# Kernel optimization log

Hardware: AMD Instinct MI355X
Metric: run time of the kernel (lower is better)

Reference implementation:

```python
import jax, jax.numpy as jnp
import numpy as np
import math

HIDDEN = 512
NUM_HEADS = 8
HEAD_DIM = HIDDEN // NUM_HEADS
NUM_BUCKETS = 32
MAX_DISTANCE = 128


def _relative_position_bucket(rel_pos, bidirectional=True):
    # rel_pos: int32 [S, T]
    num_buckets = NUM_BUCKETS
    ret = 0
    if bidirectional:
        num_buckets //= 2
        ret = (rel_pos > 0).astype(jnp.int32) * num_buckets
        rel_pos = jnp.abs(rel_pos)
    else:
        rel_pos = -jnp.minimum(rel_pos, 0)
    max_exact = num_buckets // 2
    is_small = rel_pos < max_exact
    # guard log(0); result unused where is_small
    safe = jnp.maximum(rel_pos, 1).astype(jnp.float32)
    val_if_large = max_exact + (
        jnp.log(safe / max_exact) / math.log(MAX_DISTANCE / max_exact) * (num_buckets - max_exact)
    ).astype(jnp.int32)
    val_if_large = jnp.minimum(val_if_large, num_buckets - 1)
    return ret + jnp.where(is_small, rel_pos, val_if_large)


def setup_inputs() -> dict:
    key = jax.random.key(0)
    ks = jax.random.split(key, 6)
    B, S = 4, 2048
    std = 1.0 / math.sqrt(HIDDEN)
    inp = {
        "x": jax.random.normal(ks[0], (B, S, HIDDEN), dtype=jnp.float32),
        "Wq": jax.random.normal(ks[1], (HIDDEN, HIDDEN), dtype=jnp.float32) * std,
        "Wk": jax.random.normal(ks[2], (HIDDEN, HIDDEN), dtype=jnp.float32) * std,
        "Wv": jax.random.normal(ks[3], (HIDDEN, HIDDEN), dtype=jnp.float32) * std,
        "Wo": jax.random.normal(ks[4], (HIDDEN, HIDDEN), dtype=jnp.float32) * std,
        "bias_table": jax.random.normal(ks[5], (NUM_BUCKETS, NUM_HEADS), dtype=jnp.float32) * 0.02,
    }
    return inp


def reference(x, Wq, Wk, Wv, Wo, bias_table):
    # x: [B, S, HIDDEN]; weights: [HIDDEN, HIDDEN] (out = x @ W.T semantics folded as x @ W here
    # -- weights are random so orientation is a convention; we use x @ W).
    B, S, _ = x.shape
    T = S  # self-attention, context=None
    scale = HEAD_DIM ** -0.5

    def split_heads(t, L):
        return t.reshape(B, L, NUM_HEADS, HEAD_DIM).transpose(0, 2, 1, 3)  # [B,H,L,D]

    q = split_heads(x @ Wq, S)
    k = split_heads(x @ Wk, T)
    v = split_heads(x @ Wv, T)

    # relative position bias: [1, H, S, T]
    rel = jnp.arange(T, dtype=jnp.int32)[None, :] - jnp.arange(S, dtype=jnp.int32)[:, None]
    buckets = _relative_position_bucket(rel, bidirectional=True)  # [S, T]
    pos_bias = bias_table[buckets]  # [S, T, H]
    pos_bias = pos_bias.transpose(2, 0, 1)[None]  # [1, H, S, T]

    attn = jnp.einsum("bhsd,bhtd->bhst", q, k) * scale + pos_bias
    attn = jax.nn.softmax(attn, axis=-1)  # dropout = identity (eval)
    out = jnp.einsum("bhst,bhtd->bhsd", attn, v)
    out = out.transpose(0, 2, 1, 3).reshape(B, S, HIDDEN)
    return out @ Wo
```

## Files before the change

kernel.cpp:

```cpp
#include <hip/hip_runtime.h>
#include <hip/hip_bf16.h>
#include <math.h>

#define HIDDEN 512
#define NHEADS 8
#define HDIM 64
#define SLEN 2048
#define BATCH 4
#define NROWS (BATCH*SLEN)
#define RTAB (2*SLEN-1)
#define LOG2E 1.44269504088896340736f
#define SCALE_L2E (0.125f * LOG2E)

typedef _Float16 f16;
typedef f16 f16x8 __attribute__((ext_vector_type(8)));
typedef float f32x4 __attribute__((ext_vector_type(4)));
typedef unsigned short u16;
typedef unsigned int u32;
typedef u16 u16x4 __attribute__((ext_vector_type(4)));
typedef u16 u16x8 __attribute__((ext_vector_type(8)));
typedef u32 u32x4 __attribute__((ext_vector_type(4)));

__global__ __launch_bounds__(256) void bias_precompute(
    const float* __restrict__ bias_table, float* __restrict__ biasrel) {
  int i = blockIdx.x * 256 + threadIdx.x;
  if (i >= NHEADS * RTAB) return;
  int h = i / RTAB;
  int idx = i - h * RTAB;
  int rel = idx - (SLEN - 1);
  int ret = rel > 0 ? 16 : 0;
  int a = rel < 0 ? -rel : rel;
  int bidx;
  if (a < 8) {
    bidx = a;
  } else {
    float val = logf((float)a * 0.125f) / logf(16.0f) * 8.0f;
    bidx = 8 + (int)val;
    if (bidx > 15) bidx = 15;
  }
  biasrel[i] = bias_table[(ret + bidx) * NHEADS + h] * LOG2E;
}

__global__ __launch_bounds__(256) void conv_x(
    const float* __restrict__ x, u16* __restrict__ xh) {
  int i = blockIdx.x * 256 + threadIdx.x;
  const float4* p = (const float4*)(x + (size_t)i * 8);
  float4 a = p[0], b = p[1];
  u16x8 o;
  f16 t0 = (f16)a.x; o[0] = *(u16*)&t0;
  f16 t1 = (f16)a.y; o[1] = *(u16*)&t1;
  f16 t2 = (f16)a.z; o[2] = *(u16*)&t2;
  f16 t3 = (f16)a.w; o[3] = *(u16*)&t3;
  f16 t4 = (f16)b.x; o[4] = *(u16*)&t4;
  f16 t5 = (f16)b.y; o[5] = *(u16*)&t5;
  f16 t6 = (f16)b.z; o[6] = *(u16*)&t6;
  f16 t7 = (f16)b.w; o[7] = *(u16*)&t7;
  *(u16x8*)(xh + (size_t)i * 8) = o;
}

__global__ __launch_bounds__(256) void conv_w(
    const float* __restrict__ Wq, const float* __restrict__ Wk,
    const float* __restrict__ Wv, const float* __restrict__ Wo,
    u16* __restrict__ Wt) {
  const float* W = blockIdx.y == 0 ? Wq : blockIdx.y == 1 ? Wk
                 : blockIdx.y == 2 ? Wv : Wo;
  u16* dst = Wt + (size_t)blockIdx.y * HIDDEN * HIDDEN;
  int t = blockIdx.x * 256 + threadIdx.x;
  int k = t >> 6, n0 = (t & 63) << 3;
  const float4* p = (const float4*)(W + (size_t)k * HIDDEN + n0);
  float4 a = p[0], b = p[1];
  float vals[8] = {a.x, a.y, a.z, a.w, b.x, b.y, b.z, b.w};
#pragma unroll
  for (int j = 0; j < 8; ++j) {
    f16 hv = (f16)vals[j];
    dst[(size_t)(n0 + j) * HIDDEN + k] = *(u16*)&hv;
  }
}

__global__ __launch_bounds__(256) void gemm_mfma(
    const u16* __restrict__ A, const u16* __restrict__ Wt0,
    const u16* __restrict__ Wt1, const u16* __restrict__ Wt2,
    void* __restrict__ O, int mode) {
  __shared__ u16 sm[2 * 128 * 72];
  u16 (*As)[72] = (u16(*)[72])sm;
  u16 (*Bs)[72] = (u16(*)[72])(sm + 128 * 72);
  const u16* Wt = blockIdx.z == 0 ? Wt0 : blockIdx.z == 1 ? Wt1 : Wt2;
  const int tid = threadIdx.x;
  const int w = tid >> 6, l = tid & 63;
  const int lr = l & 15, lg = l >> 4;
  const int wr = w >> 1, wc = w & 1;
  const int m0 = blockIdx.x << 7, n0 = blockIdx.y << 7;
  const int vtmode = (mode == 1) && (blockIdx.z == 2);

  f32x4 acc[4][4] = {};

  u16x8 areg[4], breg[4];
#pragma unroll
  for (int e = 0; e < 4; ++e) {
    int c = (e << 8) + tid;
    int row = c >> 3, g = c & 7;
    areg[e] = *(const u16x8*)(A + (size_t)(m0 + row) * HIDDEN + (g << 3));
    breg[e] = *(const u16x8*)(Wt + (size_t)(n0 + row) * HIDDEN + (g << 3));
  }

  for (int k0 = 0; k0 < HIDDEN; k0 += 64) {
    __syncthreads();
#pragma unroll
    for (int e = 0; e < 4; ++e) {
      int c = (e << 8) + tid;
      int row = c >> 3, g = c & 7;
      *(u16x8*)&As[row][g << 3] = areg[e];
      *(u16x8*)&Bs[row][g << 3] = breg[e];
    }
    __syncthreads();
    if (k0 + 64 < HIDDEN) {
#pragma unroll
      for (int e = 0; e < 4; ++e) {
        int c = (e << 8) + tid;
        int row = c >> 3, g = c & 7;
        areg[e] = *(const u16x8*)(A + (size_t)(m0 + row) * HIDDEN + k0 + 64 + (g << 3));
        breg[e] = *(const u16x8*)(Wt + (size_t)(n0 + row) * HIDDEN + k0 + 64 + (g << 3));
      }
    }
#pragma unroll
    for (int kk = 0; kk < 64; kk += 32) {
      f16x8 af[4], bf[4];
#pragma unroll
      for (int mt = 0; mt < 4; ++mt)
        af[mt] = *(const f16x8*)&As[(wr << 6) + (mt << 4) + lr][kk + (lg << 3)];
#pragma unroll
      for (int nt = 0; nt < 4; ++nt)
        bf[nt] = *(const f16x8*)&Bs[(wc << 6) + (nt << 4) + lr][kk + (lg << 3)];
      if (!vtmode) {
#pragma unroll
        for (int mt = 0; mt < 4; ++mt)
#pragma unroll
          for (int nt = 0; nt < 4; ++nt)
            acc[mt][nt] = __builtin_amdgcn_mfma_f32_16x16x32_f16(
                af[mt], bf[nt], acc[mt][nt], 0, 0, 0);
      } else {
#pragma unroll
        for (int i = 0; i < 4; ++i)
#pragma unroll
          for (int j = 0; j < 4; ++j)
            acc[i][j] = __builtin_amdgcn_mfma_f32_16x16x32_f16(
                bf[i], af[j], acc[i][j], 0, 0, 0);
      }
    }
  }

  if (mode == 0) {
    float* Of = (float*)O;
#pragma unroll
    for (int mt = 0; mt < 4; ++mt)
#pragma unroll
      for (int nt = 0; nt < 4; ++nt)
#pragma unroll
        for (int r = 0; r < 4; ++r) {
          int m = m0 + (wr << 6) + (mt << 4) + (lg << 2) + r;
          int n = n0 + (wc << 6) + (nt << 4) + lr;
          Of[(size_t)m * HIDDEN + n] = acc[mt][nt][r];
        }
  } else if (!vtmode) {
    u16* O16 = (u16*)O + (size_t)blockIdx.z * NROWS * HIDDEN;
    const float osc = (blockIdx.z == 0) ? SCALE_L2E : 1.0f;
#pragma unroll
    for (int mt = 0; mt < 4; ++mt)
#pragma unroll
      for (int nt = 0; nt < 4; ++nt)
#pragma unroll
        for (int r = 0; r < 4; ++r) {
          int m = m0 + (wr << 6) + (mt << 4) + (lg << 2) + r;
          int n = n0 + (wc << 6) + (nt << 4) + lr;
          int b = m >> 11, s = m & (SLEN - 1);
          int h = n >> 6, d = n & 63;
          f16 hv = (f16)(acc[mt][nt][r] * osc);
          O16[(((size_t)b * NHEADS + h) * SLEN + s) * HDIM + d] = *(u16*)&hv;
        }
  } else {
    __syncthreads();
    u16* tt = sm;
#pragma unroll
    for (int i = 0; i < 4; ++i)
#pragma unroll
      for (int j = 0; j < 4; ++j)
#pragma unroll
        for (int r = 0; r < 4; ++r) {
          int nl = (wc << 6) + (i << 4) + (lg << 2) + r;
          int ml = (wr << 6) + (j << 4) + lr;
          f16 hv = (f16)acc[i][j][r];
          tt[nl * 136 + ml] = *(u16*)&hv;
        }
    __syncthreads();
    u16* O16 = (u16*)O + (size_t)2 * NROWS * HIDDEN;
    int nl = tid >> 1, half = tid & 1;
    int n = n0 + nl;
    int h = n >> 6, d = n & 63;
    int b = m0 >> 11, s_base = m0 & (SLEN - 1);
    u16* orow = O16 + (((size_t)b * NHEADS + h) * HDIM + d) * SLEN + s_base;
    const u16* trow = tt + nl * 136;
#pragma unroll
    for (int c = 0; c < 8; ++c) {
      int v_off = (half << 6) + (c << 3);
      int c0 = (v_off & ~31) | (((v_off >> 3) & 3) << 2);
      u16x4 lo = *(const u16x4*)(trow + c0);
      u16x4 hi = *(const u16x4*)(trow + c0 + 16);
      u16x8 st;
#pragma unroll
      for (int j = 0; j < 4; ++j) { st[j] = lo[j]; st[j + 4] = hi[j]; }
      *(u16x8*)(orow + v_off) = st;
    }
  }
}

__global__ __launch_bounds__(256) void flash_attn_mfma(
    const u16* __restrict__ qg, const u16* __restrict__ kg,
    const u16* __restrict__ vtg, const float* __restrict__ biasrel,
    u16* __restrict__ attn_out) {
  __shared__ u16 Ks[64][72];
  __shared__ u16 Vt[64][72];

  const int tid = threadIdx.x;
  const int w = tid >> 6, l = tid & 63;
  const int lr = l & 15, lg = l >> 4;

  int bid = blockIdx.x;
  int xcd = bid & 7, idx = bid >> 3;
  int bh = (xcd << 2) + (idx >> 4);
  int bx = idx & 15;
  int h = bh & 7, b = bh >> 3;
  int q0 = bx << 7;

  const u16* qp = qg + (size_t)bh * (SLEN * HDIM);
  const u16* kp = kg + (size_t)bh * (SLEN * HDIM);
  const u16* vp = vtg + (size_t)bh * (HDIM * SLEN);

  const float bias_pos = biasrel[h * RTAB + 2 * (SLEN - 1)];
  const float bias_neg = biasrel[h * RTAB];

  f16x8 aq[2][2];
#pragma unroll
  for (int sub = 0; sub < 2; ++sub) {
    const u16* qrow = qp + (size_t)(q0 + (w << 5) + (sub << 4) + lr) * HDIM + (lg << 3);
    aq[sub][0] = *(const f16x8*)(qrow);
    aq[sub][1] = *(const f16x8*)(qrow + 32);
  }

  const float* bb = biasrel + h * RTAB + (SLEN - 1) + (lg << 2) - lr - q0 - (w << 5);

  f32x4 acc[2][4] = {};
  float l_run[2] = {0.f, 0.f};

  u16x8 kreg[2], vreg[2];
#pragma unroll
  for (int e = 0; e < 2; ++e) {
    int c = tid + (e << 8);
    int row = c >> 3, c8 = (c & 7) << 3;
    kreg[e] = *(const u16x8*)(kp + (size_t)row * HDIM + c8);
    vreg[e] = *(const u16x8*)(vp + (size_t)row * SLEN + c8);
  }

  for (int t0 = 0; t0 < SLEN; t0 += 64) {
    __syncthreads();
#pragma unroll
    for (int e = 0; e < 2; ++e) {
      int c = tid + (e << 8);
      int row = c >> 3, c8 = (c & 7) << 3;
      *(u16x8*)&Ks[row][c8] = kreg[e];
      *(u16x8*)&Vt[row][c8] = vreg[e];
    }
    __syncthreads();

    if (t0 + 64 < SLEN) {
#pragma unroll
      for (int e = 0; e < 2; ++e) {
        int c = tid + (e << 8);
        int row = c >> 3, c8 = (c & 7) << 3;
        kreg[e] = *(const u16x8*)(kp + (size_t)(t0 + 64 + row) * HDIM + c8);
        vreg[e] = *(const u16x8*)(vp + (size_t)row * SLEN + t0 + 64 + c8);
      }
    }

    int dtq = t0 - q0;
    f32x4 sc[2][4];
    if (dtq >= 256 || dtq <= -192) {
      float c = (dtq > 0) ? bias_pos : bias_neg;
      f32x4 cv = {c, c, c, c};
#pragma unroll
      for (int sub = 0; sub < 2; ++sub)
#pragma unroll
        for (int ct = 0; ct < 4; ++ct) sc[sub][ct] = cv;
    } else {
#pragma unroll
      for (int sub = 0; sub < 2; ++sub)
#pragma unroll
        for (int ct = 0; ct < 4; ++ct)
#pragma unroll
          for (int r = 0; r < 4; ++r)
            sc[sub][ct][r] = bb[t0 + (ct << 4) + r - (sub << 4)];
    }

    f16x8 kf[4][2];
#pragma unroll
    for (int ct = 0; ct < 4; ++ct) {
      kf[ct][0] = *(const f16x8*)&Ks[(ct << 4) + lr][lg << 3];
      kf[ct][1] = *(const f16x8*)&Ks[(ct << 4) + lr][32 + (lg << 3)];
    }

    __builtin_amdgcn_s_setprio(1);
#pragma unroll
    for (int sub = 0; sub < 2; ++sub)
#pragma unroll
      for (int ct = 0; ct < 4; ++ct) {
        sc[sub][ct] = __builtin_amdgcn_mfma_f32_16x16x32_f16(
            kf[ct][0], aq[sub][0], sc[sub][ct], 0, 0, 0);
        sc[sub][ct] = __builtin_amdgcn_mfma_f32_16x16x32_f16(
            kf[ct][1], aq[sub][1], sc[sub][ct], 0, 0, 0);
      }
    __builtin_amdgcn_s_setprio(0);

#pragma unroll
    for (int sub = 0; sub < 2; ++sub) {
      float rs = 0.f;
#pragma unroll
      for (int ct = 0; ct < 4; ++ct)
#pragma unroll
        for (int r = 0; r < 4; ++r) {
          float pe = __builtin_amdgcn_exp2f(sc[sub][ct][r]);
          sc[sub][ct][r] = pe;
          rs += pe;
        }
      l_run[sub] += rs;
    }

    f16x8 vf[2][4];
#pragma unroll
    for (int kb = 0; kb < 2; ++kb)
#pragma unroll
      for (int dt = 0; dt < 4; ++dt)
        vf[kb][dt] = *(const f16x8*)&Vt[(dt << 4) + lr][(kb << 5) + (lg << 3)];

    __builtin_amdgcn_s_setprio(1);
#pragma unroll
    for (int sub = 0; sub < 2; ++sub)
#pragma unroll
      for (int kb = 0; kb < 2; ++kb) {
        u32 a0 = __builtin_bit_cast(u32,
            __builtin_amdgcn_cvt_pkrtz(sc[sub][2 * kb][0], sc[sub][2 * kb][1]));
        u32 a1 = __builtin_bit_cast(u32,
            __builtin_amdgcn_cvt_pkrtz(sc[sub][2 * kb][2], sc[sub][2 * kb][3]));
        u32 a2 = __builtin_bit_cast(u32,
            __builtin_amdgcn_cvt_pkrtz(sc[sub][2 * kb + 1][0], sc[sub][2 * kb + 1][1]));
        u32 a3 = __builtin_bit_cast(u32,
            __builtin_amdgcn_cvt_pkrtz(sc[sub][2 * kb + 1][2], sc[sub][2 * kb + 1][3]));
        u32x4 pk = {a0, a1, a2, a3};
        f16x8 pa = __builtin_bit_cast(f16x8, pk);
#pragma unroll
        for (int dt = 0; dt < 4; ++dt)
          acc[sub][dt] = __builtin_amdgcn_mfma_f32_16x16x32_f16(
              pa, vf[kb][dt], acc[sub][dt], 0, 0, 0);
      }
    __builtin_amdgcn_s_setprio(0);
  }

#pragma unroll
  for (int sub = 0; sub < 2; ++sub) {
    float lt = l_run[sub];
    lt += __shfl_xor(lt, 16, 64);
    lt += __shfl_xor(lt, 32, 64);
    float linv[4];
#pragma unroll
    for (int r = 0; r < 4; ++r) linv[r] = 1.f / __shfl(lt, (lg << 2) + r, 16);
    u16* op = attn_out +
              ((size_t)(b * SLEN) + q0 + (w << 5) + (sub << 4)) * HIDDEN + (h << 6);
#pragma unroll
    for (int r = 0; r < 4; ++r)
#pragma unroll
      for (int dt = 0; dt < 4; ++dt) {
        f16 hv = (f16)(acc[sub][dt][r] * linv[r]);
        op[(size_t)((lg << 2) + r) * HIDDEN + (dt << 4) + lr] = *(u16*)&hv;
      }
  }
}

extern "C" void kernel_launch(void* const* d_in, const int* in_sizes, int n_in,
                              void* d_out, int out_size, void* d_ws, size_t ws_size,
                              hipStream_t stream) {
  const float* x          = (const float*)d_in[0];
  const float* Wq         = (const float*)d_in[1];
  const float* Wk         = (const float*)d_in[2];
  const float* Wv         = (const float*)d_in[3];
  const float* Wo         = (const float*)d_in[4];
  const float* bias_table = (const float*)d_in[5];
  float* out = (float*)d_out;

  u16* xh   = (u16*)d_ws;
  u16* wt   = xh + (size_t)NROWS * HIDDEN;
  u16* qkv  = wt + (size_t)4 * HIDDEN * HIDDEN;
  u16* attno_h = qkv + (size_t)3 * NROWS * HIDDEN;
  float* biasrel = (float*)(attno_h + (size_t)NROWS * HIDDEN);

  u16* qb = qkv;
  u16* kb = qkv + (size_t)NROWS * HIDDEN;
  u16* vb = qkv + (size_t)2 * NROWS * HIDDEN;

  bias_precompute<<<(NHEADS * RTAB + 255) / 256, 256, 0, stream>>>(bias_table, biasrel);
  conv_x<<<NROWS * HIDDEN / 8 / 256, 256, 0, stream>>>(x, xh);
  conv_w<<<dim3(HIDDEN * HIDDEN / 8 / 256, 4), 256, 0, stream>>>(Wq, Wk, Wv, Wo, wt);

  u16* wtq = wt;
  u16* wtk = wt + (size_t)HIDDEN * HIDDEN;
  u16* wtv = wt + (size_t)2 * HIDDEN * HIDDEN;
  u16* wto = wt + (size_t)3 * HIDDEN * HIDDEN;

  gemm_mfma<<<dim3(NROWS / 128, HIDDEN / 128, 3), 256, 0, stream>>>(
      xh, wtq, wtk, wtv, qkv, 1);

  flash_attn_mfma<<<SLEN / 128 * BATCH * NHEADS, 256, 0, stream>>>(
      qb, kb, vb, biasrel, attno_h);

  gemm_mfma<<<dim3(NROWS / 128, HIDDEN / 128, 1), 256, 0, stream>>>(
      attno_h, wto, wto, wto, out, 0);
}
```

Measured before the change: 105.3 us.

## Fuse x conversion into QKV GEMM, stage epilogue via LDS, double-buffer attention K/V

Removes the separate fp32-to-fp16 conversion kernel for x: the QKV GEMM now loads fp32 x and packs it with cvt_pkrtz on the fly. The Q scale is folded into the weight conversion. The Q/K epilogue is staged through shared memory so head-major stores are 16-byte vectors instead of scattered 2-byte writes. The flash attention K/V tiles are double-buffered in LDS, leaving one barrier per iteration. In exchange the QKV GEMM reads twice the A bytes from global memory across three z-slices, and attention uses more LDS per block.

```diff
diff --git a/kernel.cpp b/kernel.cpp
--- a/kernel.cpp
+++ b/kernel.cpp
@@ -20,6 +20,15 @@
 typedef u16 u16x4 __attribute__((ext_vector_type(4)));
 typedef u16 u16x8 __attribute__((ext_vector_type(8)));
 typedef u32 u32x4 __attribute__((ext_vector_type(4)));
+
+__device__ __forceinline__ u16x8 pack8(float4 a, float4 b) {
+  u32 p0 = __builtin_bit_cast(u32, __builtin_amdgcn_cvt_pkrtz(a.x, a.y));
+  u32 p1 = __builtin_bit_cast(u32, __builtin_amdgcn_cvt_pkrtz(a.z, a.w));
+  u32 p2 = __builtin_bit_cast(u32, __builtin_amdgcn_cvt_pkrtz(b.x, b.y));
+  u32 p3 = __builtin_bit_cast(u32, __builtin_amdgcn_cvt_pkrtz(b.z, b.w));
+  u32x4 r = {p0, p1, p2, p3};
+  return __builtin_bit_cast(u16x8, r);
+}
 
 __global__ __launch_bounds__(256) void bias_precompute(
     const float* __restrict__ bias_table, float* __restrict__ biasrel) {
@@ -41,29 +50,13 @@
   biasrel[i] = bias_table[(ret + bidx) * NHEADS + h] * LOG2E;
 }
 
-__global__ __launch_bounds__(256) void conv_x(
-    const float* __restrict__ x, u16* __restrict__ xh) {
-  int i = blockIdx.x * 256 + threadIdx.x;
-  const float4* p = (const float4*)(x + (size_t)i * 8);
-  float4 a = p[0], b = p[1];
-  u16x8 o;
-  f16 t0 = (f16)a.x; o[0] = *(u16*)&t0;
-  f16 t1 = (f16)a.y; o[1] = *(u16*)&t1;
-  f16 t2 = (f16)a.z; o[2] = *(u16*)&t2;
-  f16 t3 = (f16)a.w; o[3] = *(u16*)&t3;
-  f16 t4 = (f16)b.x; o[4] = *(u16*)&t4;
-  f16 t5 = (f16)b.y; o[5] = *(u16*)&t5;
-  f16 t6 = (f16)b.z; o[6] = *(u16*)&t6;
-  f16 t7 = (f16)b.w; o[7] = *(u16*)&t7;
-  *(u16x8*)(xh + (size_t)i * 8) = o;
-}
-
 __global__ __launch_bounds__(256) void conv_w(
     const float* __restrict__ Wq, const float* __restrict__ Wk,
     const float* __restrict__ Wv, const float* __restrict__ Wo,
     u16* __restrict__ Wt) {
   const float* W = blockIdx.y == 0 ? Wq : blockIdx.y == 1 ? Wk
                  : blockIdx.y == 2 ? Wv : Wo;
+  const float sc = (blockIdx.y == 0) ? SCALE_L2E : 1.0f;
   u16* dst = Wt + (size_t)blockIdx.y * HIDDEN * HIDDEN;
   int t = blockIdx.x * 256 + threadIdx.x;
   int k = t >> 6, n0 = (t & 63) << 3;
@@ -72,18 +65,20 @@
   float vals[8] = {a.x, a.y, a.z, a.w, b.x, b.y, b.z, b.w};
 #pragma unroll
   for (int j = 0; j < 8; ++j) {
-    f16 hv = (f16)vals[j];
+    f16 hv = (f16)(vals[j] * sc);
     dst[(size_t)(n0 + j) * HIDDEN + k] = *(u16*)&hv;
   }
 }
 
 __global__ __launch_bounds__(256) void gemm_mfma(
-    const u16* __restrict__ A, const u16* __restrict__ Wt0,
+    const void* __restrict__ Ap, const u16* __restrict__ Wt0,
     const u16* __restrict__ Wt1, const u16* __restrict__ Wt2,
     void* __restrict__ O, int mode) {
   __shared__ u16 sm[2 * 128 * 72];
   u16 (*As)[72] = (u16(*)[72])sm;
   u16 (*Bs)[72] = (u16(*)[72])(sm + 128 * 72);
+  const u16* A16 = (const u16*)Ap;
+  const float* A32 = (const float*)Ap;
   const u16* Wt = blockIdx.z == 0 ? Wt0 : blockIdx.z == 1 ? Wt1 : Wt2;
   const int tid = threadIdx.x;
   const int w = tid >> 6, l = tid & 63;
@@ -99,7 +94,12 @@
   for (int e = 0; e < 4; ++e) {
     int c = (e << 8) + tid;
     int row = c >> 3, g = c & 7;
-    areg[e] = *(const u16x8*)(A + (size_t)(m0 + row) * HIDDEN + (g << 3));
+    if (mode == 1) {
+      const float* ap = A32 + (size_t)(m0 + row) * HIDDEN + (g << 3);
+      areg[e] = pack8(*(const float4*)ap, *(const float4*)(ap + 4));
+    } else {
+      areg[e] = *(const u16x8*)(A16 + (size_t)(m0 + row) * HIDDEN + (g << 3));
+    }
     breg[e] = *(const u16x8*)(Wt + (size_t)(n0 + row) * HIDDEN + (g << 3));
   }
 
@@ -118,7 +118,12 @@
       for (int e = 0; e < 4; ++e) {
         int c = (e << 8) + tid;
         int row = c >> 3, g = c & 7;
-        areg[e] = *(const u16x8*)(A + (size_t)(m0 + row) * HIDDEN + k0 + 64 + (g << 3));
+        if (mode == 1) {
+          const float* ap = A32 + (size_t)(m0 + row) * HIDDEN + k0 + 64 + (g << 3);
+          areg[e] = pack8(*(const float4*)ap, *(const float4*)(ap + 4));
+        } else {
+          areg[e] = *(const u16x8*)(A16 + (size_t)(m0 + row) * HIDDEN + k0 + 64 + (g << 3));
+        }
         breg[e] = *(const u16x8*)(Wt + (size_t)(n0 + row) * HIDDEN + k0 + 64 + (g << 3));
       }
     }
@@ -162,21 +167,32 @@
           Of[(size_t)m * HIDDEN + n] = acc[mt][nt][r];
         }
   } else if (!vtmode) {
+    __syncthreads();
+    u16* tt = sm;
+#pragma unroll
+    for (int mt = 0; mt < 4; ++mt)
+#pragma unroll
+      for (int nt = 0; nt < 4; ++nt)
+#pragma unroll
+        for (int r = 0; r < 4; ++r) {
+          int ml = (wr << 6) + (mt << 4) + (lg << 2) + r;
+          int nl = (wc << 6) + (nt << 4) + lr;
+          f16 hv = (f16)acc[mt][nt][r];
+          tt[ml * 136 + nl] = *(u16*)&hv;
+        }
+    __syncthreads();
     u16* O16 = (u16*)O + (size_t)blockIdx.z * NROWS * HIDDEN;
-    const float osc = (blockIdx.z == 0) ? SCALE_L2E : 1.0f;
-#pragma unroll
-    for (int mt = 0; mt < 4; ++mt)
-#pragma unroll
-      for (int nt = 0; nt < 4; ++nt)
-#pragma unroll
-        for (int r = 0; r < 4; ++r) {
-          int m = m0 + (wr << 6) + (mt << 4) + (lg << 2) + r;
-          int n = n0 + (wc << 6) + (nt << 4) + lr;
-          int b = m >> 11, s = m & (SLEN - 1);
-          int h = n >> 6, d = n & 63;
-          f16 hv = (f16)(acc[mt][nt][r] * osc);
-          O16[(((size_t)b * NHEADS + h) * SLEN + s) * HDIM + d] = *(u16*)&hv;
-        }
+    int b = m0 >> 11, s0 = m0 & (SLEN - 1);
+    int hl = tid >> 7, rr = tid & 127;
+    int hh = (n0 >> 6) + hl;
+    u16* obase = O16 + (((size_t)b * NHEADS + hh) * SLEN + s0) * HDIM;
+#pragma unroll
+    for (int c = 0; c < 8; ++c) {
+      int sl = (rr >> 3) + (c << 4);
+      int d8 = (rr & 7) << 3;
+      u16x8 v = *(const u16x8*)&tt[sl * 136 + (hl << 6) + d8];
+      *(u16x8*)(obase + (size_t)sl * HDIM + d8) = v;
+    }
   } else {
     __syncthreads();
     u16* tt = sm;
@@ -217,8 +233,8 @@
     const u16* __restrict__ qg, const u16* __restrict__ kg,
     const u16* __restrict__ vtg, const float* __restrict__ biasrel,
     u16* __restrict__ attn_out) {
-  __shared__ u16 Ks[64][72];
-  __shared__ u16 Vt[64][72];
+  __shared__ u16 Ks[2][64][72];
+  __shared__ u16 Vt[2][64][72];
 
   const int tid = threadIdx.x;
   const int w = tid >> 6, l = tid & 63;
@@ -259,25 +275,40 @@
     kreg[e] = *(const u16x8*)(kp + (size_t)row * HDIM + c8);
     vreg[e] = *(const u16x8*)(vp + (size_t)row * SLEN + c8);
   }
-
+#pragma unroll
+  for (int e = 0; e < 2; ++e) {
+    int c = tid + (e << 8);
+    int row = c >> 3, c8 = (c & 7) << 3;
+    *(u16x8*)&Ks[0][row][c8] = kreg[e];
+    *(u16x8*)&Vt[0][row][c8] = vreg[e];
+  }
+#pragma unroll
+  for (int e = 0; e < 2; ++e) {
+    int c = tid + (e << 8);
+    int row = c >> 3, c8 = (c & 7) << 3;
+    kreg[e] = *(const u16x8*)(kp + (size_t)(64 + row) * HDIM + c8);
+    vreg[e] = *(const u16x8*)(vp + (size_t)row * SLEN + 64 + c8);
+  }
+  __syncthreads();
+
+  int cur = 0;
   for (int t0 = 0; t0 < SLEN; t0 += 64) {
-    __syncthreads();
-#pragma unroll
-    for (int e = 0; e < 2; ++e) {
-      int c = tid + (e << 8);
-      int row = c >> 3, c8 = (c & 7) << 3;
-      *(u16x8*)&Ks[row][c8] = kreg[e];
-      *(u16x8*)&Vt[row][c8] = vreg[e];
-    }
-    __syncthreads();
-
     if (t0 + 64 < SLEN) {
 #pragma unroll
       for (int e = 0; e < 2; ++e) {
         int c = tid + (e << 8);
         int row = c >> 3, c8 = (c & 7) << 3;
-        kreg[e] = *(const u16x8*)(kp + (size_t)(t0 + 64 + row) * HDIM + c8);
-        vreg[e] = *(const u16x8*)(vp + (size_t)row * SLEN + t0 + 64 + c8);
+        *(u16x8*)&Ks[cur ^ 1][row][c8] = kreg[e];
+        *(u16x8*)&Vt[cur ^ 1][row][c8] = vreg[e];
+      }
+      if (t0 + 128 < SLEN) {
+#pragma unroll
+        for (int e = 0; e < 2; ++e) {
+          int c = tid + (e << 8);
+          int row = c >> 3, c8 = (c & 7) << 3;
+          kreg[e] = *(const u16x8*)(kp + (size_t)(t0 + 128 + row) * HDIM + c8);
+          vreg[e] = *(const u16x8*)(vp + (size_t)row * SLEN + t0 + 128 + c8);
+        }
       }
     }
 
@@ -303,8 +334,8 @@
     f16x8 kf[4][2];
 #pragma unroll
     for (int ct = 0; ct < 4; ++ct) {
-      kf[ct][0] = *(const f16x8*)&Ks[(ct << 4) + lr][lg << 3];
-      kf[ct][1] = *(const f16x8*)&Ks[(ct << 4) + lr][32 + (lg << 3)];
+      kf[ct][0] = *(const f16x8*)&Ks[cur][(ct << 4) + lr][lg << 3];
+      kf[ct][1] = *(const f16x8*)&Ks[cur][(ct << 4) + lr][32 + (lg << 3)];
     }
 
     __builtin_amdgcn_s_setprio(1);
@@ -338,7 +369,7 @@
     for (int kb = 0; kb < 2; ++kb)
 #pragma unroll
       for (int dt = 0; dt < 4; ++dt)
-        vf[kb][dt] = *(const f16x8*)&Vt[(dt << 4) + lr][(kb << 5) + (lg << 3)];
+        vf[kb][dt] = *(const f16x8*)&Vt[cur][(dt << 4) + lr][(kb << 5) + (lg << 3)];
 
     __builtin_amdgcn_s_setprio(1);
 #pragma unroll
@@ -361,6 +392,9 @@
               pa, vf[kb][dt], acc[sub][dt], 0, 0, 0);
       }
     __builtin_amdgcn_s_setprio(0);
+
+    __syncthreads();
+    cur ^= 1;
   }
 
 #pragma unroll
@@ -394,8 +428,7 @@
   const float* bias_table = (const float*)d_in[5];
   float* out = (float*)d_out;
 
-  u16* xh   = (u16*)d_ws;
-  u16* wt   = xh + (size_t)NROWS * HIDDEN;
+  u16* wt   = (u16*)d_ws;
   u16* qkv  = wt + (size_t)4 * HIDDEN * HIDDEN;
   u16* attno_h = qkv + (size_t)3 * NROWS * HIDDEN;
   float* biasrel = (float*)(attno_h + (size_t)NROWS * HIDDEN);
@@ -405,7 +438,6 @@
   u16* vb = qkv + (size_t)2 * NROWS * HIDDEN;
 
   bias_precompute<<<(NHEADS * RTAB + 255) / 256, 256, 0, stream>>>(bias_table, biasrel);
-  conv_x<<<NROWS * HIDDEN / 8 / 256, 256, 0, stream>>>(x, xh);
   conv_w<<<dim3(HIDDEN * HIDDEN / 8 / 256, 4), 256, 0, stream>>>(Wq, Wk, Wv, Wo, wt);
 
   u16* wtq = wt;
@@ -414,7 +446,7 @@
   u16* wto = wt + (size_t)3 * HIDDEN * HIDDEN;
 
   gemm_mfma<<<dim3(NROWS / 128, HIDDEN / 128, 3), 256, 0, stream>>>(
-      xh, wtq, wtk, wtv, qkv, 1);
+      x, wtq, wtk, wtv, qkv, 1);
 
   flash_attn_mfma<<<SLEN / 128 * BATCH * NHEADS, 256, 0, stream>>>(
       qb, kb, vb, biasrel, attno_h);
```

New measurement: 127.5 us. 1.21x slower.

## Double-buffer K/V tiles in LDS to drop one barrier per iteration

Applied to the files above, without the earlier changes.

Adds a second LDS buffer for the K and V tiles. Each iteration writes the next tile into the alternate buffer while computing on the current one, which leaves one __syncthreads per iteration instead of two. The global prefetch now runs two tiles ahead. In exchange the LDS footprint doubles (about 36 KB per block), which may reduce occupancy, and register-held prefetch data has to live longer.

```diff
diff --git a/kernel.cpp b/kernel.cpp
--- a/kernel.cpp
+++ b/kernel.cpp
@@ -217,8 +217,8 @@
     const u16* __restrict__ qg, const u16* __restrict__ kg,
     const u16* __restrict__ vtg, const float* __restrict__ biasrel,
     u16* __restrict__ attn_out) {
-  __shared__ u16 Ks[64][72];
-  __shared__ u16 Vt[64][72];
+  __shared__ u16 Ks[2][64][72];
+  __shared__ u16 Vt[2][64][72];
 
   const int tid = threadIdx.x;
   const int w = tid >> 6, l = tid & 63;
@@ -259,25 +259,40 @@
     kreg[e] = *(const u16x8*)(kp + (size_t)row * HDIM + c8);
     vreg[e] = *(const u16x8*)(vp + (size_t)row * SLEN + c8);
   }
-
+#pragma unroll
+  for (int e = 0; e < 2; ++e) {
+    int c = tid + (e << 8);
+    int row = c >> 3, c8 = (c & 7) << 3;
+    *(u16x8*)&Ks[0][row][c8] = kreg[e];
+    *(u16x8*)&Vt[0][row][c8] = vreg[e];
+  }
+#pragma unroll
+  for (int e = 0; e < 2; ++e) {
+    int c = tid + (e << 8);
+    int row = c >> 3, c8 = (c & 7) << 3;
+    kreg[e] = *(const u16x8*)(kp + (size_t)(64 + row) * HDIM + c8);
+    vreg[e] = *(const u16x8*)(vp + (size_t)row * SLEN + 64 + c8);
+  }
+  __syncthreads();
+
+  int cur = 0;
   for (int t0 = 0; t0 < SLEN; t0 += 64) {
-    __syncthreads();
-#pragma unroll
-    for (int e = 0; e < 2; ++e) {
-      int c = tid + (e << 8);
-      int row = c >> 3, c8 = (c & 7) << 3;
-      *(u16x8*)&Ks[row][c8] = kreg[e];
-      *(u16x8*)&Vt[row][c8] = vreg[e];
-    }
-    __syncthreads();
-
     if (t0 + 64 < SLEN) {
 #pragma unroll
       for (int e = 0; e < 2; ++e) {
         int c = tid + (e << 8);
         int row = c >> 3, c8 = (c & 7) << 3;
-        kreg[e] = *(const u16x8*)(kp + (size_t)(t0 + 64 + row) * HDIM + c8);
-        vreg[e] = *(const u16x8*)(vp + (size_t)row * SLEN + t0 + 64 + c8);
+        *(u16x8*)&Ks[cur ^ 1][row][c8] = kreg[e];
+        *(u16x8*)&Vt[cur ^ 1][row][c8] = vreg[e];
+      }
+      if (t0 + 128 < SLEN) {
+#pragma unroll
+        for (int e = 0; e < 2; ++e) {
+          int c = tid + (e << 8);
+          int row = c >> 3, c8 = (c & 7) << 3;
+          kreg[e] = *(const u16x8*)(kp + (size_t)(t0 + 128 + row) * HDIM + c8);
+          vreg[e] = *(const u16x8*)(vp + (size_t)row * SLEN + t0 + 128 + c8);
+        }
       }
     }
 
@@ -303,8 +318,8 @@
     f16x8 kf[4][2];
 #pragma unroll
     for (int ct = 0; ct < 4; ++ct) {
-      kf[ct][0] = *(const f16x8*)&Ks[(ct << 4) + lr][lg << 3];
-      kf[ct][1] = *(const f16x8*)&Ks[(ct << 4) + lr][32 + (lg << 3)];
+      kf[ct][0] = *(const f16x8*)&Ks[cur][(ct << 4) + lr][lg << 3];
+      kf[ct][1] = *(const f16x8*)&Ks[cur][(ct << 4) + lr][32 + (lg << 3)];
     }
 
     __builtin_amdgcn_s_setprio(1);
@@ -338,7 +353,7 @@
     for (int kb = 0; kb < 2; ++kb)
 #pragma unroll
       for (int dt = 0; dt < 4; ++dt)
-        vf[kb][dt] = *(const f16x8*)&Vt[(dt << 4) + lr][(kb << 5) + (lg << 3)];
+        vf[kb][dt] = *(const f16x8*)&Vt[cur][(dt << 4) + lr][(kb << 5) + (lg << 3)];
 
     __builtin_amdgcn_s_setprio(1);
 #pragma unroll
@@ -361,6 +376,9 @@
               pa, vf[kb][dt], acc[sub][dt], 0, 0, 0);
       }
     __builtin_amdgcn_s_setprio(0);
+
+    __syncthreads();
+    cur ^= 1;
   }
 
 #pragma unroll
```

After: 105.6 us. Within noise of the previous version (+0.3%).
